# Kernel optimization log

Hardware: AMD Instinct MI355X
Metric: run time of the kernel (lower is better)

Reference implementation:

```python
import jax, jax.numpy as jnp
import numpy as np

L, H, A, NREL2 = 3, 64, 64, 474
N_NODE, N_EDGE, B = 100000, 1000000, 32


def setup_inputs() -> dict:
    key = jax.random.key(0)
    ks = jax.random.split(key, 20)
    f = jax.random.normal
    s = 0.05
    return dict(
        sub_idx=jax.random.randint(ks[0], (N_EDGE,), 0, N_NODE),
        rel_idx=jax.random.randint(ks[1], (N_EDGE,), 0, NREL2),
        obj_idx=jax.random.randint(ks[2], (N_EDGE,), 0, N_NODE),
        edge_batch=jax.random.randint(ks[3], (N_EDGE,), 0, B),
        q_rel=jax.random.randint(ks[4], (B,), 0, NREL2),
        query_sub_idxs=jax.random.randint(ks[5], (B,), 0, N_NODE),
        rela_embed=f(ks[6], (L, NREL2, H)) * s,
        query_rela_embed=f(ks[7], (NREL2, H)) * s,
        Ws=f(ks[8], (L, H, A)) * s,
        Wr=f(ks[9], (L, H, A)) * s,
        Wqr=f(ks[10], (L, H, A)) * s,
        bqr=f(ks[11], (L, A)) * s,
        w_alpha=f(ks[12], (L, A)) * s,
        b_alpha=f(ks[13], (L,)) * s,
        W_h=f(ks[14], (L, H, H)) * s,
        gru_Wih=f(ks[15], (L, 3 * H, H)) * s,
        gru_Whh=f(ks[16], (L, 3 * H, H)) * s,
        gru_bih=f(ks[17], (L, 3 * H)) * s,
        gru_bhh=f(ks[18], (L, 3 * H)) * s,
        W_final=f(ks[19], (H,)) * s,
        n_node=N_NODE,
    )


def reference(sub_idx, rel_idx, obj_idx, edge_batch, q_rel, query_sub_idxs,
              rela_embed, query_rela_embed, Ws, Wr, Wqr, bqr, w_alpha, b_alpha,
              W_h, gru_Wih, gru_Whh, gru_bih, gru_bhh, W_final, n_node):
    # initializer='relation': seed query-subject nodes with query relation embedding
    hidden = jnp.zeros((n_node, H), jnp.float32).at[query_sub_idxs].set(query_rela_embed[q_rel])
    h0 = jnp.zeros((n_node, H), jnp.float32)  # GRU state

    for l in range(L):
        # ---- GNNLayer: gather -> attention MLP -> scatter-add ----
        hs = hidden[sub_idx]                       # [E, H]
        hr = rela_embed[l][rel_idx]                # [E, H]
        h_qr = rela_embed[l][q_rel][edge_batch]    # [E, H] query-rel emb per edge
        pre = jax.nn.relu(hs @ Ws[l] + hr @ Wr[l] + h_qr @ Wqr[l] + bqr[l])  # [E, A]
        alpha = jax.nn.sigmoid(pre @ w_alpha[l] + b_alpha[l])[:, None]       # [E, 1]
        msg = alpha * (hs * hr)                                              # [E, H]
        agg = jax.ops.segment_sum(msg, obj_idx, num_segments=n_node)        # [N, H]
        hidden = jax.nn.relu(agg @ W_h[l])

        # act_signal: mask untouched nodes (detached in original)
        mask = jnp.where(jax.lax.stop_gradient(jnp.sum(hidden, -1)) == 0, 0.0, 1.0)[:, None]

        # ---- one GRU step per node (PyTorch GRU math) ----
        gi = hidden @ gru_Wih[l].T + gru_bih[l]   # [N, 3H]
        gh = h0 @ gru_Whh[l].T + gru_bhh[l]       # [N, 3H]
        i_r, i_z, i_n = jnp.split(gi, 3, axis=-1)
        h_r, h_z, h_n = jnp.split(gh, 3, axis=-1)
        r = jax.nn.sigmoid(i_r + h_r)
        z = jax.nn.sigmoid(i_z + h_z)
        n = jnp.tanh(i_n + r * h_n)
        h_new = (1.0 - z) * n + z * h0
        hidden = h_new * mask
        h0 = h_new * mask

    # readout='linear', no bias
    scores = hidden @ W_final                     # [N]
    return scores
```

## Files before the change

kernel.cpp:

```cpp
#include <hip/hip_runtime.h>
#include <hip/hip_bf16.h>

#define NL 3
#define HD 64
#define TCAP 2048
#define NB 8

typedef unsigned char u8;

__device__ __forceinline__ float sigf(float x){ return 1.f/(1.f+__expf(-x)); }

__device__ __forceinline__ float wsum(float v){
  #pragma unroll
  for (int off=32; off; off>>=1) v += __shfl_xor(v, off, 64);
  return v;
}

__device__ __forceinline__ float bcastf(float v, int l){
  return __int_as_float(__builtin_amdgcn_readlane(__float_as_int(v), l));
}

__device__ __forceinline__ float ldin(const void* p, size_t i, int bf){
  return bf ? __bfloat162float(((const __hip_bfloat16*)p)[i]) : ((const float*)p)[i];
}

__global__ void k_dtype(const unsigned short* __restrict__ probe, int* __restrict__ flag){
  int lane = threadIdx.x & 63;
  unsigned short h = probe[lane];
  int e = (h >> 7) & 0xFF;
  int sane = ((h & 0x7FFF) == 0) || (e >= 96 && e <= 132);
  unsigned long long m = __ballot(sane != 0);
  if (lane == 0) flag[0] = (__popcll(m) >= 56) ? 1 : 0;
}

__global__ void k_prep(
    const void* __restrict__ W_h, const void* __restrict__ Ws,
    const void* __restrict__ Wih, const void* __restrict__ Whh,
    const void* __restrict__ bih, const void* __restrict__ bhh,
    const void* __restrict__ wal, const void* __restrict__ bal,
    const void* __restrict__ Wf,  const void* __restrict__ rel,
    float* __restrict__ WhF, float* __restrict__ WsF,
    float* __restrict__ WiT, float* __restrict__ WhT,
    float* __restrict__ biF, float* __restrict__ bhF,
    float* __restrict__ waF, float* __restrict__ baF,
    float* __restrict__ WfF, float* __restrict__ REL,
    const int* __restrict__ flag, int NR)
{
  int bf = flag[0];
  int j = blockIdx.x*256 + threadIdx.x;
  const int sWT = NL*HD*HD, sWI = NL*192*HD, sB = NL*192;
  if (j < sWT){ WhF[j]=ldin(W_h,j,bf); return; } j-=sWT;
  if (j < sWT){ WsF[j]=ldin(Ws ,j,bf); return; } j-=sWT;
  if (j < sWI){ int l=j/(192*HD), q=j%(192*HD), h=q/192, a=q%192;
                WiT[j]=ldin(Wih,(size_t)l*192*HD + (size_t)a*HD + h,bf); return; } j-=sWI;
  if (j < sWI){ int l=j/(192*HD), q=j%(192*HD), h=q/192, a=q%192;
                WhT[j]=ldin(Whh,(size_t)l*192*HD + (size_t)a*HD + h,bf); return; } j-=sWI;
  if (j < sB){ biF[j]=ldin(bih,j,bf); return; } j-=sB;
  if (j < sB){ bhF[j]=ldin(bhh,j,bf); return; } j-=sB;
  if (j < NL*HD){ waF[j]=ldin(wal,j,bf); return; } j-=NL*HD;
  if (j < NL){ baF[j]=ldin(bal,j,bf); return; } j-=NL;
  if (j < HD){ WfF[j]=ldin(Wf,j,bf); return; } j-=HD;
  if (j < NL*NR*HD){ REL[j]=ldin(rel,j,bf); return; }
}

__global__ void k_tables(
    const void* __restrict__ rel, const void* __restrict__ Wr,
    const void* __restrict__ Wqr, const void* __restrict__ bqr,
    const int* __restrict__ q_rel,
    float* __restrict__ R2, float* __restrict__ QR,
    const int* __restrict__ flag, int NR, int B)
{
  int bf = flag[0];
  int lane = threadIdx.x & 63;
  int bid = blockIdx.x;
  if (bid < NL*NR){
    int l = bid/NR, r = bid%NR;
    float x = ldin(rel,(size_t)(l*NR+r)*HD + lane,bf);
    float acc = 0.f;
    #pragma unroll
    for (int h=0; h<HD; ++h)
      acc = fmaf(bcastf(x, h), ldin(Wr,(size_t)(l*HD+h)*HD + lane,bf), acc);
    R2[(size_t)bid*HD + lane] = acc;
  } else {
    int b2 = bid - NL*NR;
    int l = b2/B, b = b2%B;
    int r = q_rel[b];
    float x = ldin(rel,(size_t)(l*NR+r)*HD + lane,bf);
    float acc = ldin(bqr,(size_t)l*HD + lane,bf);
    #pragma unroll
    for (int h=0; h<HD; ++h)
      acc = fmaf(bcastf(x, h), ldin(Wqr,(size_t)(l*HD+h)*HD + lane,bf), acc);
    QR[(size_t)b2*HD + lane] = acc;
  }
}

__global__ void k_init(
    const int* __restrict__ qsub, const int* __restrict__ q_rel,
    const void* __restrict__ qre, const float* __restrict__ WsF0,
    float* __restrict__ hid, float* __restrict__ HS2, u8* __restrict__ liveB,
    int* __restrict__ stamp, int* __restrict__ plist, int* __restrict__ pcnt,
    const int* __restrict__ flag, int B)
{
  int bf = flag[0];
  int lane = threadIdx.x & 63;
  int b = blockIdx.x;
  int n = qsub[b];
  for (int b2 = b+1; b2 < B; ++b2) if (qsub[b2] == n) return;
  int r = q_rel[b];
  float v = ldin(qre,(size_t)r*HD + lane,bf);
  hid[(size_t)n*HD + lane] = v;
  float acc = 0.f;
  #pragma unroll 8
  for (int h=0; h<HD; ++h)
    acc = fmaf(bcastf(v,h), WsF0[h*HD + lane], acc);
  HS2[(size_t)n*HD + lane] = acc;
  if (lane==0){
    liveB[n] = 1;
    stamp[n] = 1;
    int idx = atomicAdd(pcnt, 1);
    plist[idx] = n;
  }
}

__global__ void __launch_bounds__(256) k_edge(
    const int* __restrict__ sub, const int* __restrict__ rel_i,
    const int* __restrict__ obj, const int* __restrict__ eb,
    const u8* __restrict__ liveB,
    const float* __restrict__ hid, const float* __restrict__ HS2,
    const float* __restrict__ R2l, const float* __restrict__ QRl,
    const float* __restrict__ RELl, const float* __restrict__ waFl,
    const float* __restrict__ baFl, float* __restrict__ agg,
    int* __restrict__ stamp, int* __restrict__ tlist, int* __restrict__ tcnt,
    int ep, int E)
{
  __shared__ int s_cnt;
  __shared__ int s_base;
  __shared__ int s_buf[TCAP];
  if (threadIdx.x == 0) s_cnt = 0;
  __syncthreads();

  int lane = threadIdx.x & 63;
  int wid = (blockIdx.x*256 + threadIdx.x) >> 6;
  int nw = gridDim.x*4;
  float wa = waFl[lane];
  float ba = baFl[0];

  for (long long base = (long long)wid*256; base < E; base += (long long)nw*256){
    unsigned long long m[4];
    if (base + 256 <= E){
      int4 s4 = *reinterpret_cast<const int4*>(&sub[base + 4*(long long)lane]);
      bool l0 = liveB[s4.x] != 0;
      bool l1 = liveB[s4.y] != 0;
      bool l2 = liveB[s4.z] != 0;
      bool l3 = liveB[s4.w] != 0;
      m[0] = __ballot(l0); m[1] = __ballot(l1);
      m[2] = __ballot(l2); m[3] = __ballot(l3);
    } else {
      #pragma unroll
      for (int j=0;j<4;++j){
        long long e = base + 4*(long long)lane + j;
        bool lv = (e < E) && (liveB[sub[e]] != 0);
        m[j] = __ballot(lv);
      }
    }
    #pragma unroll
    for (int j=0;j<4;++j){
      unsigned long long mask = m[j];
      while (mask){
        int bit = (int)__ffsll(mask) - 1;
        mask &= mask - 1;
        long long ee = base + 4*(long long)bit + j;
        int ss = sub[ee], r = rel_i[ee], o = obj[ee], b = eb[ee];
        float hs  = hid[(size_t)ss*HD + lane];
        float pre = HS2[(size_t)ss*HD + lane] + R2l[(size_t)r*HD + lane] + QRl[(size_t)b*HD + lane];
        pre = fmaxf(pre, 0.f);
        float d = wsum(pre*wa) + ba;
        float alpha = sigf(d);
        float msg = alpha * hs * RELl[(size_t)r*HD + lane];
        unsafeAtomicAdd(&agg[(size_t)o*HD + lane], msg);
        if (lane==0){
          int old = atomicExch(&stamp[o], ep);
          if (old != ep){
            int li = atomicAdd(&s_cnt, 1);
            if (li < TCAP) s_buf[li] = o;
            else { int gi = atomicAdd(tcnt, 1); tlist[gi] = o; }
          }
        }
      }
    }
  }

  __syncthreads();
  int cnt = s_cnt; if (cnt > TCAP) cnt = TCAP;
  if (threadIdx.x == 0 && cnt > 0) s_base = atomicAdd(tcnt, cnt);
  __syncthreads();
  if (cnt > 0){
    int b0 = s_base;
    for (int i = threadIdx.x; i < cnt; i += 256) tlist[b0 + i] = s_buf[i];
  }
}

__global__ void __launch_bounds__(256) k_node(
    const int* __restrict__ tlist, const int* __restrict__ tcnt,
    float* __restrict__ agg, float* __restrict__ hid, float* __restrict__ HS2,
    u8* __restrict__ liveB,
    const float* __restrict__ WhFl,
    const float* __restrict__ WiTl,
    const float* __restrict__ WhTl,
    const float* __restrict__ biFl, const float* __restrict__ bhFl,
    const float* __restrict__ WsFn,
    const float* __restrict__ WfF,
    float* __restrict__ out, int N, int isFirst, int isLast)
{
  int cntv = tcnt[0]; if (cntv > N) cntv = N;
  int lane = threadIdx.x & 63;
  int wid = (blockIdx.x*256 + threadIdx.x) >> 6;
  int nw = gridDim.x*4;
  float bi0=biFl[lane], bi1=biFl[HD+lane], bi2=biFl[2*HD+lane];
  float bh0=bhFl[lane], bh1=bhFl[HD+lane], bh2=bhFl[2*HD+lane];
  float wfv = isLast ? WfF[lane] : 0.f;

  for (int i0 = wid*NB; i0 < cntv; i0 += nw*NB){
    int nd[NB]; bool val[NB]; bool wp[NB]; float av[NB];
    #pragma unroll
    for (int j=0;j<NB;++j){
      val[j] = (i0+j) < cntv;
      nd[j]  = tlist[val[j] ? (i0+j) : i0];
      wp[j]  = (!isFirst) && val[j] && (liveB[nd[j]] != 0);
      av[j]  = val[j] ? agg[(size_t)nd[j]*HD + lane] : 0.f;
    }
    if (!isLast){
      #pragma unroll
      for (int j=0;j<NB;++j) if (val[j]) agg[(size_t)nd[j]*HD + lane] = 0.f;
    }

    float hm[NB];
    #pragma unroll
    for (int j=0;j<NB;++j) hm[j] = 0.f;
    #pragma unroll 8
    for (int h=0; h<HD; ++h){
      float w = WhFl[h*HD + lane];
      #pragma unroll
      for (int j=0;j<NB;++j) hm[j] = fmaf(bcastf(av[j],h), w, hm[j]);
    }
    float mask[NB]; float h0v[NB];
    #pragma unroll
    for (int j=0;j<NB;++j){
      hm[j] = fmaxf(hm[j], 0.f);
      mask[j] = (__ballot(hm[j] != 0.f) != 0ull) ? 1.f : 0.f;
      h0v[j] = wp[j] ? hid[(size_t)nd[j]*HD + lane] : 0.f;
    }

    float gi0[NB], gi1[NB], gi2[NB], gh0[NB], gh1[NB], gh2[NB];
    #pragma unroll
    for (int j=0;j<NB;++j){ gi0[j]=bi0; gi1[j]=bi1; gi2[j]=bi2; gh0[j]=bh0; gh1[j]=bh1; gh2[j]=bh2; }
    #pragma unroll 4
    for (int h=0; h<HD; ++h){
      const float* __restrict__ wr = WiTl + (size_t)h*192;
      float w0 = wr[lane], w1 = wr[64+lane], w2 = wr[128+lane];
      #pragma unroll
      for (int j=0;j<NB;++j){
        float x = bcastf(hm[j],h);
        gi0[j] = fmaf(x, w0, gi0[j]);
        gi1[j] = fmaf(x, w1, gi1[j]);
        gi2[j] = fmaf(x, w2, gi2[j]);
      }
    }
    #pragma unroll
    for (int j=0;j<NB;++j){
      if (wp[j]){
        #pragma unroll 4
        for (int h=0; h<HD; ++h){
          const float* __restrict__ wr = WhTl + (size_t)h*192;
          float y = bcastf(h0v[j],h);
          gh0[j] = fmaf(y, wr[lane],     gh0[j]);
          gh1[j] = fmaf(y, wr[64+lane],  gh1[j]);
          gh2[j] = fmaf(y, wr[128+lane], gh2[j]);
        }
      }
    }

    float hn[NB];
    #pragma unroll
    for (int j=0;j<NB;++j){
      float r = sigf(gi0[j]+gh0[j]);
      float z = sigf(gi1[j]+gh1[j]);
      float nn = tanhf(gi2[j] + r*gh2[j]);
      hn[j] = ((1.f - z)*nn + z*h0v[j])*mask[j];
    }

    if (isLast){
      #pragma unroll
      for (int j=0;j<NB;++j){
        float sc = wsum(hn[j] * wfv);
        if (lane==0 && val[j]) out[nd[j]] = sc;
      }
      continue;
    }
    #pragma unroll
    for (int j=0;j<NB;++j){
      unsigned long long lv = __ballot(hn[j] != 0.f);
      if (val[j]){
        hid[(size_t)nd[j]*HD + lane] = hn[j];
        if (lane==0) liveB[nd[j]] = lv ? (u8)1 : (u8)0;
      }
    }

    float acc[NB];
    #pragma unroll
    for (int j=0;j<NB;++j) acc[j] = 0.f;
    #pragma unroll 8
    for (int h=0; h<HD; ++h){
      float w = WsFn[h*HD + lane];
      #pragma unroll
      for (int j=0;j<NB;++j) acc[j] = fmaf(bcastf(hn[j],h), w, acc[j]);
    }
    #pragma unroll
    for (int j=0;j<NB;++j) if (val[j]) HS2[(size_t)nd[j]*HD + lane] = acc[j];
  }
}

__global__ void k_died(const int* __restrict__ plist, const int* __restrict__ pcnt,
                       const int* __restrict__ stamp, u8* __restrict__ liveB, int ep, int N)
{
  int cntv = pcnt[0]; if (cntv > N) cntv = N;
  int t = blockIdx.x*256 + threadIdx.x;
  for (int i = t; i < cntv; i += gridDim.x*256){
    int n = plist[i];
    if (stamp[n] != ep) liveB[n] = 0;
  }
}

extern "C" void kernel_launch(void* const* d_in, const int* in_sizes, int n_in,
                              void* d_out, int out_size, void* d_ws, size_t ws_size,
                              hipStream_t stream)
{
  const int* sub   = (const int*)d_in[0];
  const int* rel_i = (const int*)d_in[1];
  const int* obj   = (const int*)d_in[2];
  const int* eb    = (const int*)d_in[3];
  const int* q_rel = (const int*)d_in[4];
  const int* qsub  = (const int*)d_in[5];
  const void* rela = d_in[6];
  const void* qre  = d_in[7];
  const void* Wsp  = d_in[8];
  const void* Wr   = d_in[9];
  const void* Wqr  = d_in[10];
  const void* bqr  = d_in[11];
  const void* wal  = d_in[12];
  const void* bal  = d_in[13];
  const void* W_h  = d_in[14];
  const void* Wih  = d_in[15];
  const void* Whh  = d_in[16];
  const void* bih  = d_in[17];
  const void* bhh  = d_in[18];
  const void* Wf   = d_in[19];

  int E  = in_sizes[0];
  int B  = in_sizes[4];
  int NR = in_sizes[6]/(NL*HD);
  int N  = out_size;

  float* ws = (float*)d_ws;
  size_t o = 0;
  float* agg  = ws + o; o += (size_t)N*HD;
  float* hid  = ws + o; o += (size_t)N*HD;
  float* HS2  = ws + o; o += (size_t)N*HD;
  float* R2   = ws + o; o += (size_t)NL*NR*HD;
  float* QR   = ws + o; o += (size_t)NL*B*HD;
  float* REL  = ws + o; o += (size_t)NL*NR*HD;
  float* WhF  = ws + o; o += NL*HD*HD;
  float* WsF  = ws + o; o += NL*HD*HD;
  float* WiT  = ws + o; o += NL*192*HD;
  float* WhT  = ws + o; o += NL*192*HD;
  float* biF  = ws + o; o += NL*192;
  float* bhF  = ws + o; o += NL*192;
  float* waF  = ws + o; o += NL*HD;
  float* baF  = ws + o; o += NL;
  float* WfF  = ws + o; o += HD;
  int*   listA= (int*)(ws + o); o += N;
  int*   listB= (int*)(ws + o); o += N;
  int*   stamp= (int*)(ws + o); o += N;
  int*   cnts = (int*)(ws + o); o += 16;
  u8*    liveB= (u8*)(ws + o);

  hipMemsetAsync(agg,   0, (size_t)N*HD*sizeof(float), stream);
  hipMemsetAsync(stamp, 0, (size_t)N*sizeof(int) + 16*sizeof(int) + (size_t)N, stream);
  hipMemsetAsync(d_out, 0, (size_t)N*sizeof(float), stream);

  k_dtype<<<1, 64, 0, stream>>>((const unsigned short*)rela, cnts+8);

  int prepN = 2*(NL*HD*HD) + 2*(NL*192*HD) + 2*(NL*192) + NL*HD + NL + HD + NL*NR*HD;
  k_prep<<<(prepN+255)/256, 256, 0, stream>>>(W_h, Wsp, Wih, Whh, bih, bhh, wal, bal, Wf, rela,
      WhF, WsF, WiT, WhT, biF, bhF, waF, baF, WfF, REL, cnts+8, NR);
  k_tables<<<NL*NR + NL*B, 64, 0, stream>>>(rela, Wr, Wqr, bqr, q_rel, R2, QR, cnts+8, NR, B);
  k_init<<<B, 64, 0, stream>>>(qsub, q_rel, qre, WsF, hid, HS2, liveB,
                               stamp, listA, cnts+3, cnts+8, B);

  int* curT = listB;
  int* prevL = listA;
  for (int l=0; l<NL; ++l){
    int ep = l + 2;
    k_edge<<<1024, 256, 0, stream>>>(sub, rel_i, obj, eb, liveB, hid, HS2,
        R2 + (size_t)l*NR*HD, QR + (size_t)l*B*HD, REL + (size_t)l*NR*HD,
        waF + l*HD, baF + l, agg, stamp, curT, cnts+4+l, ep, E);
    k_node<<<2048, 256, 0, stream>>>(curT, cnts+4+l, agg, hid, HS2, liveB,
        WhF + (size_t)l*HD*HD, WiT + (size_t)l*192*HD, WhT + (size_t)l*192*HD,
        biF + l*192, bhF + l*192,
        (l < NL-1) ? (WsF + (size_t)(l+1)*HD*HD) : WsF,
        WfF, (float*)d_out, N, (l==0)?1:0, (l==NL-1)?1:0);
    if (l < NL-1){
      k_died<<<64, 256, 0, stream>>>(prevL, (l==0) ? (cnts+3) : (cnts+4+l-1),
                                     stamp, liveB, ep, N);
    }
    int* t = prevL; prevL = curT; curT = t;
  }
}
```

Baseline: 188.1 us.

## Fuse setup kernels, merge memsets, fold dead-node pass into node kernel

The dtype probe, weight prep, relation tables and init kernels are merged into one launch, with each block computing the dtype flag inline. Workspace is reordered so agg, stamp, counters and liveB are zeroed by a single memset. The per-layer k_died pass moves into the tail of k_node. k_node now stages W_h and Wih in shared memory and runs on 512 blocks instead of 2048. The aim is fewer launches and less global weight traffic, at the cost of a larger shared-memory footprint per block and less parallelism in k_node.

Result: no change. 188.1 us (+0.0%).

```diff
diff --git a/kernel.cpp b/kernel.cpp
--- a/kernel.cpp
+++ b/kernel.cpp
@@ -24,86 +24,78 @@
   return bf ? __bfloat162float(((const __hip_bfloat16*)p)[i]) : ((const float*)p)[i];
 }
 
-__global__ void k_dtype(const unsigned short* __restrict__ probe, int* __restrict__ flag){
-  int lane = threadIdx.x & 63;
-  unsigned short h = probe[lane];
+__device__ __forceinline__ int probe_bf(const void* probe, int lane){
+  unsigned short h = ((const unsigned short*)probe)[lane];
   int e = (h >> 7) & 0xFF;
   int sane = ((h & 0x7FFF) == 0) || (e >= 96 && e <= 132);
   unsigned long long m = __ballot(sane != 0);
-  if (lane == 0) flag[0] = (__popcll(m) >= 56) ? 1 : 0;
-}
-
-__global__ void k_prep(
+  return (__popcll(m) >= 56) ? 1 : 0;
+}
+
+__global__ void __launch_bounds__(256) k_setup(
     const void* __restrict__ W_h, const void* __restrict__ Ws,
     const void* __restrict__ Wih, const void* __restrict__ Whh,
     const void* __restrict__ bih, const void* __restrict__ bhh,
     const void* __restrict__ wal, const void* __restrict__ bal,
     const void* __restrict__ Wf,  const void* __restrict__ rel,
+    const void* __restrict__ Wr,  const void* __restrict__ Wqr,
+    const void* __restrict__ bqr, const void* __restrict__ qre,
+    const int* __restrict__ q_rel, const int* __restrict__ qsub,
     float* __restrict__ WhF, float* __restrict__ WsF,
     float* __restrict__ WiT, float* __restrict__ WhT,
     float* __restrict__ biF, float* __restrict__ bhF,
     float* __restrict__ waF, float* __restrict__ baF,
     float* __restrict__ WfF, float* __restrict__ REL,
-    const int* __restrict__ flag, int NR)
-{
-  int bf = flag[0];
-  int j = blockIdx.x*256 + threadIdx.x;
-  const int sWT = NL*HD*HD, sWI = NL*192*HD, sB = NL*192;
-  if (j < sWT){ WhF[j]=ldin(W_h,j,bf); return; } j-=sWT;
-  if (j < sWT){ WsF[j]=ldin(Ws ,j,bf); return; } j-=sWT;
-  if (j < sWI){ int l=j/(192*HD), q=j%(192*HD), h=q/192, a=q%192;
-                WiT[j]=ldin(Wih,(size_t)l*192*HD + (size_t)a*HD + h,bf); return; } j-=sWI;
-  if (j < sWI){ int l=j/(192*HD), q=j%(192*HD), h=q/192, a=q%192;
-                WhT[j]=ldin(Whh,(size_t)l*192*HD + (size_t)a*HD + h,bf); return; } j-=sWI;
-  if (j < sB){ biF[j]=ldin(bih,j,bf); return; } j-=sB;
-  if (j < sB){ bhF[j]=ldin(bhh,j,bf); return; } j-=sB;
-  if (j < NL*HD){ waF[j]=ldin(wal,j,bf); return; } j-=NL*HD;
-  if (j < NL){ baF[j]=ldin(bal,j,bf); return; } j-=NL;
-  if (j < HD){ WfF[j]=ldin(Wf,j,bf); return; } j-=HD;
-  if (j < NL*NR*HD){ REL[j]=ldin(rel,j,bf); return; }
-}
-
-__global__ void k_tables(
-    const void* __restrict__ rel, const void* __restrict__ Wr,
-    const void* __restrict__ Wqr, const void* __restrict__ bqr,
-    const int* __restrict__ q_rel,
     float* __restrict__ R2, float* __restrict__ QR,
-    const int* __restrict__ flag, int NR, int B)
-{
-  int bf = flag[0];
-  int lane = threadIdx.x & 63;
-  int bid = blockIdx.x;
-  if (bid < NL*NR){
-    int l = bid/NR, r = bid%NR;
-    float x = ldin(rel,(size_t)(l*NR+r)*HD + lane,bf);
-    float acc = 0.f;
-    #pragma unroll
-    for (int h=0; h<HD; ++h)
-      acc = fmaf(bcastf(x, h), ldin(Wr,(size_t)(l*HD+h)*HD + lane,bf), acc);
-    R2[(size_t)bid*HD + lane] = acc;
-  } else {
-    int b2 = bid - NL*NR;
-    int l = b2/B, b = b2%B;
-    int r = q_rel[b];
-    float x = ldin(rel,(size_t)(l*NR+r)*HD + lane,bf);
-    float acc = ldin(bqr,(size_t)l*HD + lane,bf);
-    #pragma unroll
-    for (int h=0; h<HD; ++h)
-      acc = fmaf(bcastf(x, h), ldin(Wqr,(size_t)(l*HD+h)*HD + lane,bf), acc);
-    QR[(size_t)b2*HD + lane] = acc;
-  }
-}
-
-__global__ void k_init(
-    const int* __restrict__ qsub, const int* __restrict__ q_rel,
-    const void* __restrict__ qre, const float* __restrict__ WsF0,
     float* __restrict__ hid, float* __restrict__ HS2, u8* __restrict__ liveB,
     int* __restrict__ stamp, int* __restrict__ plist, int* __restrict__ pcnt,
-    const int* __restrict__ flag, int B)
+    int NR, int B, int PB, int TB)
 {
-  int bf = flag[0];
   int lane = threadIdx.x & 63;
-  int b = blockIdx.x;
+  int bf = probe_bf(rel, lane);
+
+  if ((int)blockIdx.x < PB){
+    int j = blockIdx.x*256 + threadIdx.x;
+    const int sWT = NL*HD*HD, sWI = NL*192*HD, sB = NL*192;
+    if (j < sWT){ WhF[j]=ldin(W_h,j,bf); return; } j-=sWT;
+    if (j < sWT){ WsF[j]=ldin(Ws ,j,bf); return; } j-=sWT;
+    if (j < sWI){ int l=j/(192*HD), q=j%(192*HD), h=q/192, a=q%192;
+                  WiT[j]=ldin(Wih,(size_t)l*192*HD + (size_t)a*HD + h,bf); return; } j-=sWI;
+    if (j < sWI){ int l=j/(192*HD), q=j%(192*HD), h=q/192, a=q%192;
+                  WhT[j]=ldin(Whh,(size_t)l*192*HD + (size_t)a*HD + h,bf); return; } j-=sWI;
+    if (j < sB){ biF[j]=ldin(bih,j,bf); return; } j-=sB;
+    if (j < sB){ bhF[j]=ldin(bhh,j,bf); return; } j-=sB;
+    if (j < NL*HD){ waF[j]=ldin(wal,j,bf); return; } j-=NL*HD;
+    if (j < NL){ baF[j]=ldin(bal,j,bf); return; } j-=NL;
+    if (j < HD){ WfF[j]=ldin(Wf,j,bf); return; } j-=HD;
+    if (j < NL*NR*HD){ REL[j]=ldin(rel,j,bf); return; }
+    return;
+  }
+  if ((int)blockIdx.x < PB+TB){
+    int bid = ((int)blockIdx.x - PB)*4 + (threadIdx.x>>6);
+    if (bid < NL*NR){
+      int l = bid/NR, r = bid%NR;
+      float x = ldin(rel,(size_t)(l*NR+r)*HD + lane,bf);
+      float acc = 0.f;
+      #pragma unroll
+      for (int h=0; h<HD; ++h)
+        acc = fmaf(bcastf(x, h), ldin(Wr,(size_t)(l*HD+h)*HD + lane,bf), acc);
+      R2[(size_t)bid*HD + lane] = acc;
+    } else if (bid < NL*NR + NL*B){
+      int b2 = bid - NL*NR;
+      int l = b2/B, b = b2%B;
+      int r = q_rel[b];
+      float x = ldin(rel,(size_t)(l*NR+r)*HD + lane,bf);
+      float acc = ldin(bqr,(size_t)l*HD + lane,bf);
+      #pragma unroll
+      for (int h=0; h<HD; ++h)
+        acc = fmaf(bcastf(x, h), ldin(Wqr,(size_t)(l*HD+h)*HD + lane,bf), acc);
+      QR[(size_t)b2*HD + lane] = acc;
+    }
+    return;
+  }
+  int b = ((int)blockIdx.x - PB - TB)*4 + (threadIdx.x>>6);
+  if (b >= B) return;
   int n = qsub[b];
   for (int b2 = b+1; b2 < B; ++b2) if (qsub[b2] == n) return;
   int r = q_rel[b];
@@ -112,7 +104,7 @@
   float acc = 0.f;
   #pragma unroll 8
   for (int h=0; h<HD; ++h)
-    acc = fmaf(bcastf(v,h), WsF0[h*HD + lane], acc);
+    acc = fmaf(bcastf(v,h), ldin(Ws,(size_t)h*HD + lane,bf), acc);
   HS2[(size_t)n*HD + lane] = acc;
   if (lane==0){
     liveB[n] = 1;
@@ -149,12 +141,10 @@
     unsigned long long m[4];
     if (base + 256 <= E){
       int4 s4 = *reinterpret_cast<const int4*>(&sub[base + 4*(long long)lane]);
-      bool l0 = liveB[s4.x] != 0;
-      bool l1 = liveB[s4.y] != 0;
-      bool l2 = liveB[s4.z] != 0;
-      bool l3 = liveB[s4.w] != 0;
-      m[0] = __ballot(l0); m[1] = __ballot(l1);
-      m[2] = __ballot(l2); m[3] = __ballot(l3);
+      m[0] = __ballot(liveB[s4.x] != 0);
+      m[1] = __ballot(liveB[s4.y] != 0);
+      m[2] = __ballot(liveB[s4.z] != 0);
+      m[3] = __ballot(liveB[s4.w] != 0);
     } else {
       #pragma unroll
       for (int j=0;j<4;++j){
@@ -174,10 +164,8 @@
         float hs  = hid[(size_t)ss*HD + lane];
         float pre = HS2[(size_t)ss*HD + lane] + R2l[(size_t)r*HD + lane] + QRl[(size_t)b*HD + lane];
         pre = fmaxf(pre, 0.f);
-        float d = wsum(pre*wa) + ba;
-        float alpha = sigf(d);
-        float msg = alpha * hs * RELl[(size_t)r*HD + lane];
-        unsafeAtomicAdd(&agg[(size_t)o*HD + lane], msg);
+        float alpha = sigf(wsum(pre*wa) + ba);
+        unsafeAtomicAdd(&agg[(size_t)o*HD + lane], alpha * hs * RELl[(size_t)r*HD + lane]);
         if (lane==0){
           int old = atomicExch(&stamp[o], ep);
           if (old != ep){
@@ -210,124 +198,134 @@
     const float* __restrict__ biFl, const float* __restrict__ bhFl,
     const float* __restrict__ WsFn,
     const float* __restrict__ WfF,
-    float* __restrict__ out, int N, int isFirst, int isLast)
+    const int* __restrict__ plist, const int* __restrict__ pcnt,
+    const int* __restrict__ stamp,
+    float* __restrict__ out, int N, int isFirst, int isLast, int ep)
 {
+  __shared__ float sWh[HD*HD];
+  __shared__ float sWi[HD*192];
   int cntv = tcnt[0]; if (cntv > N) cntv = N;
   int lane = threadIdx.x & 63;
   int wid = (blockIdx.x*256 + threadIdx.x) >> 6;
   int nw = gridDim.x*4;
-  float bi0=biFl[lane], bi1=biFl[HD+lane], bi2=biFl[2*HD+lane];
-  float bh0=bhFl[lane], bh1=bhFl[HD+lane], bh2=bhFl[2*HD+lane];
-  float wfv = isLast ? WfF[lane] : 0.f;
-
-  for (int i0 = wid*NB; i0 < cntv; i0 += nw*NB){
-    int nd[NB]; bool val[NB]; bool wp[NB]; float av[NB];
-    #pragma unroll
-    for (int j=0;j<NB;++j){
-      val[j] = (i0+j) < cntv;
-      nd[j]  = tlist[val[j] ? (i0+j) : i0];
-      wp[j]  = (!isFirst) && val[j] && (liveB[nd[j]] != 0);
-      av[j]  = val[j] ? agg[(size_t)nd[j]*HD + lane] : 0.f;
+
+  bool hasWork = ((int)blockIdx.x*4*NB) < cntv;
+  if (hasWork){
+    for (int i = threadIdx.x; i < HD*HD/4; i += 256)
+      ((float4*)sWh)[i] = ((const float4*)WhFl)[i];
+    for (int i = threadIdx.x; i < HD*192/4; i += 256)
+      ((float4*)sWi)[i] = ((const float4*)WiTl)[i];
+    __syncthreads();
+
+    float bi0=biFl[lane], bi1=biFl[HD+lane], bi2=biFl[2*HD+lane];
+    float bh0=bhFl[lane], bh1=bhFl[HD+lane], bh2=bhFl[2*HD+lane];
+    float wfv = isLast ? WfF[lane] : 0.f;
+
+    for (int i0 = wid*NB; i0 < cntv; i0 += nw*NB){
+      int nd[NB]; bool val[NB]; bool wp[NB]; float av[NB];
+      #pragma unroll
+      for (int j=0;j<NB;++j){
+        val[j] = (i0+j) < cntv;
+        nd[j]  = tlist[val[j] ? (i0+j) : i0];
+        wp[j]  = (!isFirst) && val[j] && (liveB[nd[j]] != 0);
+        av[j]  = val[j] ? agg[(size_t)nd[j]*HD + lane] : 0.f;
+      }
+      if (!isLast){
+        #pragma unroll
+        for (int j=0;j<NB;++j) if (val[j]) agg[(size_t)nd[j]*HD + lane] = 0.f;
+      }
+
+      float hm[NB];
+      #pragma unroll
+      for (int j=0;j<NB;++j) hm[j] = 0.f;
+      #pragma unroll 8
+      for (int h=0; h<HD; ++h){
+        float w = sWh[h*HD + lane];
+        #pragma unroll
+        for (int j=0;j<NB;++j) hm[j] = fmaf(bcastf(av[j],h), w, hm[j]);
+      }
+      float mask[NB]; float h0v[NB];
+      #pragma unroll
+      for (int j=0;j<NB;++j){
+        hm[j] = fmaxf(hm[j], 0.f);
+        mask[j] = (__ballot(hm[j] != 0.f) != 0ull) ? 1.f : 0.f;
+        h0v[j] = wp[j] ? hid[(size_t)nd[j]*HD + lane] : 0.f;
+      }
+
+      float gi0[NB], gi1[NB], gi2[NB], gh0[NB], gh1[NB], gh2[NB];
+      #pragma unroll
+      for (int j=0;j<NB;++j){ gi0[j]=bi0; gi1[j]=bi1; gi2[j]=bi2; gh0[j]=bh0; gh1[j]=bh1; gh2[j]=bh2; }
+      #pragma unroll 4
+      for (int h=0; h<HD; ++h){
+        const float* wr = sWi + h*192;
+        float w0 = wr[lane], w1 = wr[64+lane], w2 = wr[128+lane];
+        #pragma unroll
+        for (int j=0;j<NB;++j){
+          float x = bcastf(hm[j],h);
+          gi0[j] = fmaf(x, w0, gi0[j]);
+          gi1[j] = fmaf(x, w1, gi1[j]);
+          gi2[j] = fmaf(x, w2, gi2[j]);
+        }
+      }
+      #pragma unroll
+      for (int j=0;j<NB;++j){
+        if (wp[j]){
+          #pragma unroll 4
+          for (int h=0; h<HD; ++h){
+            const float* __restrict__ wr = WhTl + (size_t)h*192;
+            float y = bcastf(h0v[j],h);
+            gh0[j] = fmaf(y, wr[lane],     gh0[j]);
+            gh1[j] = fmaf(y, wr[64+lane],  gh1[j]);
+            gh2[j] = fmaf(y, wr[128+lane], gh2[j]);
+          }
+        }
+      }
+
+      float hn[NB];
+      #pragma unroll
+      for (int j=0;j<NB;++j){
+        float r = sigf(gi0[j]+gh0[j]);
+        float z = sigf(gi1[j]+gh1[j]);
+        float nn = tanhf(gi2[j] + r*gh2[j]);
+        hn[j] = ((1.f - z)*nn + z*h0v[j])*mask[j];
+      }
+
+      if (isLast){
+        #pragma unroll
+        for (int j=0;j<NB;++j){
+          float sc = wsum(hn[j] * wfv);
+          if (lane==0 && val[j]) out[nd[j]] = sc;
+        }
+        continue;
+      }
+      #pragma unroll
+      for (int j=0;j<NB;++j){
+        unsigned long long lv = __ballot(hn[j] != 0.f);
+        if (val[j]){
+          hid[(size_t)nd[j]*HD + lane] = hn[j];
+          if (lane==0) liveB[nd[j]] = lv ? (u8)1 : (u8)0;
+        }
+      }
+      float acc[NB];
+      #pragma unroll
+      for (int j=0;j<NB;++j) acc[j] = 0.f;
+      #pragma unroll 8
+      for (int h=0; h<HD; ++h){
+        float w = WsFn[h*HD + lane];
+        #pragma unroll
+        for (int j=0;j<NB;++j) acc[j] = fmaf(bcastf(hn[j],h), w, acc[j]);
+      }
+      #pragma unroll
+      for (int j=0;j<NB;++j) if (val[j]) HS2[(size_t)nd[j]*HD + lane] = acc[j];
     }
-    if (!isLast){
-      #pragma unroll
-      for (int j=0;j<NB;++j) if (val[j]) agg[(size_t)nd[j]*HD + lane] = 0.f;
+  }
+
+  if (!isLast){
+    int pc = pcnt[0]; if (pc > N) pc = N;
+    for (int i = blockIdx.x*256 + threadIdx.x; i < pc; i += gridDim.x*256){
+      int n = plist[i];
+      if (stamp[n] != ep) liveB[n] = 0;
     }
-
-    float hm[NB];
-    #pragma unroll
-    for (int j=0;j<NB;++j) hm[j] = 0.f;
-    #pragma unroll 8
-    for (int h=0; h<HD; ++h){
-      float w = WhFl[h*HD + lane];
-      #pragma unroll
-      for (int j=0;j<NB;++j) hm[j] = fmaf(bcastf(av[j],h), w, hm[j]);
-    }
-    float mask[NB]; float h0v[NB];
-    #pragma unroll
-    for (int j=0;j<NB;++j){
-      hm[j] = fmaxf(hm[j], 0.f);
-      mask[j] = (__ballot(hm[j] != 0.f) != 0ull) ? 1.f : 0.f;
-      h0v[j] = wp[j] ? hid[(size_t)nd[j]*HD + lane] : 0.f;
-    }
-
-    float gi0[NB], gi1[NB], gi2[NB], gh0[NB], gh1[NB], gh2[NB];
-    #pragma unroll
-    for (int j=0;j<NB;++j){ gi0[j]=bi0; gi1[j]=bi1; gi2[j]=bi2; gh0[j]=bh0; gh1[j]=bh1; gh2[j]=bh2; }
-    #pragma unroll 4
-    for (int h=0; h<HD; ++h){
-      const float* __restrict__ wr = WiTl + (size_t)h*192;
-      float w0 = wr[lane], w1 = wr[64+lane], w2 = wr[128+lane];
-      #pragma unroll
-      for (int j=0;j<NB;++j){
-        float x = bcastf(hm[j],h);
-        gi0[j] = fmaf(x, w0, gi0[j]);
-        gi1[j] = fmaf(x, w1, gi1[j]);
-        gi2[j] = fmaf(x, w2, gi2[j]);
-      }
-    }
-    #pragma unroll
-    for (int j=0;j<NB;++j){
-      if (wp[j]){
-        #pragma unroll 4
-        for (int h=0; h<HD; ++h){
-          const float* __restrict__ wr = WhTl + (size_t)h*192;
-          float y = bcastf(h0v[j],h);
-          gh0[j] = fmaf(y, wr[lane],     gh0[j]);
-          gh1[j] = fmaf(y, wr[64+lane],  gh1[j]);
-          gh2[j] = fmaf(y, wr[128+lane], gh2[j]);
-        }
-      }
-    }
-
-    float hn[NB];
-    #pragma unroll
-    for (int j=0;j<NB;++j){
-      float r = sigf(gi0[j]+gh0[j]);
-      float z = sigf(gi1[j]+gh1[j]);
-      float nn = tanhf(gi2[j] + r*gh2[j]);
-      hn[j] = ((1.f - z)*nn + z*h0v[j])*mask[j];
-    }
-
-    if (isLast){
-      #pragma unroll
-      for (int j=0;j<NB;++j){
-        float sc = wsum(hn[j] * wfv);
-        if (lane==0 && val[j]) out[nd[j]] = sc;
-      }
-      continue;
-    }
-    #pragma unroll
-    for (int j=0;j<NB;++j){
-      unsigned long long lv = __ballot(hn[j] != 0.f);
-      if (val[j]){
-        hid[(size_t)nd[j]*HD + lane] = hn[j];
-        if (lane==0) liveB[nd[j]] = lv ? (u8)1 : (u8)0;
-      }
-    }
-
-    float acc[NB];
-    #pragma unroll
-    for (int j=0;j<NB;++j) acc[j] = 0.f;
-    #pragma unroll 8
-    for (int h=0; h<HD; ++h){
-      float w = WsFn[h*HD + lane];
-      #pragma unroll
-      for (int j=0;j<NB;++j) acc[j] = fmaf(bcastf(hn[j],h), w, acc[j]);
-    }
-    #pragma unroll
-    for (int j=0;j<NB;++j) if (val[j]) HS2[(size_t)nd[j]*HD + lane] = acc[j];
-  }
-}
-
-__global__ void k_died(const int* __restrict__ plist, const int* __restrict__ pcnt,
-                       const int* __restrict__ stamp, u8* __restrict__ liveB, int ep, int N)
-{
-  int cntv = pcnt[0]; if (cntv > N) cntv = N;
-  int t = blockIdx.x*256 + threadIdx.x;
-  for (int i = t; i < cntv; i += gridDim.x*256){
-    int n = plist[i];
-    if (stamp[n] != ep) liveB[n] = 0;
   }
 }
 
@@ -364,6 +362,9 @@
   float* ws = (float*)d_ws;
   size_t o = 0;
   float* agg  = ws + o; o += (size_t)N*HD;
+  int*   stamp= (int*)(ws + o); o += N;
+  int*   cnts = (int*)(ws + o); o += 16;
+  u8*    liveB= (u8*)(ws + o); o += (N+3)/4;
   float* hid  = ws + o; o += (size_t)N*HD;
   float* HS2  = ws + o; o += (size_t)N*HD;
   float* R2   = ws + o; o += (size_t)NL*NR*HD;
@@ -380,22 +381,21 @@
   float* WfF  = ws + o; o += HD;
   int*   listA= (int*)(ws + o); o += N;
   int*   listB= (int*)(ws + o); o += N;
-  int*   stamp= (int*)(ws + o); o += N;
-  int*   cnts = (int*)(ws + o); o += 16;
-  u8*    liveB= (u8*)(ws + o);
-
-  hipMemsetAsync(agg,   0, (size_t)N*HD*sizeof(float), stream);
-  hipMemsetAsync(stamp, 0, (size_t)N*sizeof(int) + 16*sizeof(int) + (size_t)N, stream);
+
+  size_t z1 = (size_t)N*HD*sizeof(float) + (size_t)N*sizeof(int)
+            + 16*sizeof(int) + (size_t)((N+3)/4)*sizeof(float);
+  hipMemsetAsync(agg, 0, z1, stream);
   hipMemsetAsync(d_out, 0, (size_t)N*sizeof(float), stream);
 
-  k_dtype<<<1, 64, 0, stream>>>((const unsigned short*)rela, cnts+8);
-
   int prepN = 2*(NL*HD*HD) + 2*(NL*192*HD) + 2*(NL*192) + NL*HD + NL + HD + NL*NR*HD;
-  k_prep<<<(prepN+255)/256, 256, 0, stream>>>(W_h, Wsp, Wih, Whh, bih, bhh, wal, bal, Wf, rela,
-      WhF, WsF, WiT, WhT, biF, bhF, waF, baF, WfF, REL, cnts+8, NR);
-  k_tables<<<NL*NR + NL*B, 64, 0, stream>>>(rela, Wr, Wqr, bqr, q_rel, R2, QR, cnts+8, NR, B);
-  k_init<<<B, 64, 0, stream>>>(qsub, q_rel, qre, WsF, hid, HS2, liveB,
-                               stamp, listA, cnts+3, cnts+8, B);
+  int PB = (prepN + 255)/256;
+  int TB = (NL*NR + NL*B + 3)/4;
+  int IB = (B + 3)/4;
+  k_setup<<<PB + TB + IB, 256, 0, stream>>>(
+      W_h, Wsp, Wih, Whh, bih, bhh, wal, bal, Wf, rela, Wr, Wqr, bqr, qre,
+      q_rel, qsub,
+      WhF, WsF, WiT, WhT, biF, bhF, waF, baF, WfF, REL, R2, QR,
+      hid, HS2, liveB, stamp, listA, cnts+3, NR, B, PB, TB);
 
   int* curT = listB;
   int* prevL = listA;
@@ -404,15 +404,13 @@
     k_edge<<<1024, 256, 0, stream>>>(sub, rel_i, obj, eb, liveB, hid, HS2,
         R2 + (size_t)l*NR*HD, QR + (size_t)l*B*HD, REL + (size_t)l*NR*HD,
         waF + l*HD, baF + l, agg, stamp, curT, cnts+4+l, ep, E);
-    k_node<<<2048, 256, 0, stream>>>(curT, cnts+4+l, agg, hid, HS2, liveB,
+    k_node<<<512, 256, 0, stream>>>(curT, cnts+4+l, agg, hid, HS2, liveB,
         WhF + (size_t)l*HD*HD, WiT + (size_t)l*192*HD, WhT + (size_t)l*192*HD,
         biF + l*192, bhF + l*192,
         (l < NL-1) ? (WsF + (size_t)(l+1)*HD*HD) : WsF,
-        WfF, (float*)d_out, N, (l==0)?1:0, (l==NL-1)?1:0);
-    if (l < NL-1){
-      k_died<<<64, 256, 0, stream>>>(prevL, (l==0) ? (cnts+3) : (cnts+4+l-1),
-                                     stamp, liveB, ep, N);
-    }
+        WfF,
+        prevL, (l==0) ? (cnts+3) : (cnts+4+l-1), stamp,
+        (float*)d_out, N, (l==0)?1:0, (l==NL-1)?1:0, ep);
     int* t = prevL; prevL = curT; curT = t;
   }
 }
```
